# Kernel optimization log

Measured on AMD Instinct MI355X. Metric: run time of the kernel, lower is better.

## Reference

```python
import jax, jax.numpy as jnp
import numpy as np
import math

B, N, K, M = 8, 512, 128, 100

def _lin(k, fi, fo):
    kw, kb = jax.random.split(k)
    return (jax.random.normal(kw, (fi, fo), jnp.float32) / np.sqrt(fi).astype(np.float32),
            jax.random.normal(kb, (fo,), jnp.float32) * 0.01)

def setup_inputs() -> dict:
    key = jax.random.key(0)
    ks = jax.random.split(key, 10)
    xyz = jax.random.uniform(ks[0], (B, N, K, 3), jnp.float32, minval=0.5, maxval=2.8)
    counts = jax.random.randint(ks[1], (B, N), 32, K + 1)
    # padded neighbor list: valid neighbors first (flag=1), padding zeros after -> break == mask
    flags = (jnp.arange(K)[None, None, :] < counts[:, :, None]).astype(jnp.float32)
    image_dR = jnp.concatenate([xyz, flags[..., None]], axis=-1)  # [B,N,K,4]
    ew0, eb0 = _lin(ks[2], 1, 25)
    ew1, eb1 = _lin(ks[3], 25, 50)
    ew2, eb2 = _lin(ks[4], 50, M)
    fw0, fb0 = _lin(ks[5], 16 * M, 240)
    fw1, fb1 = _lin(ks[6], 240, 240)
    fw2, fb2 = _lin(ks[7], 240, 240)
    fw3, fb3 = _lin(ks[8], 240, 1)
    return dict(image_dR=image_dR, ew0=ew0, eb0=eb0, ew1=ew1, eb1=eb1, ew2=ew2, eb2=eb2,
                fw0=fw0, fb0=fb0, fw1=fw1, fb1=fb1, fw2=fw2, fb2=fb2, fw3=fw3, fb3=fb3)

def reference(image_dR, ew0, eb0, ew1, eb1, ew2, eb2, fw0, fb0, fw1, fb1, fw2, fb2, fw3, fb3):
    list_neigh = image_dR[..., 3]            # [B,N,K] neighbor flag
    xyz = image_dR[..., :3]                  # [B,N,K,3]
    Rij = jnp.sum(xyz * xyz, axis=-1)        # NOTE: original overwrites sqrt -> squared distance
    mask = list_neigh > 0
    lt10 = Rij < 10.0
    b1 = mask & lt10
    b2 = (~lt10) & (Rij < 25.0)              # cosine branch ignores mask (faithful)
    safe = jnp.where(Rij == 0.0, 1.0, Rij)
    S = jnp.where(b1, 1.0 / safe,
                  jnp.where(b2, 0.5 * jnp.cos(math.pi * (Rij - 10.0) / 15.0) + 0.5, 0.0))
    coef = jnp.where(mask, S / safe, 0.0)    # per-neighbor scaling for xyz channels
    Ri = jnp.concatenate([S[..., None], coef[..., None] * xyz], axis=-1)  # [B,N,K,4]
    # embedding net on scalar S_Rij
    h = jnp.tanh(S[..., None] @ ew0 + eb0)
    h = jnp.tanh(h @ ew1 + eb1)
    G = jnp.tanh(h @ ew2 + eb2)              # [B,N,K,M]
    G16 = G[..., :16]
    tmpA = jnp.einsum('bnjm,bnjf->bnmf', G16, Ri)   # [B,N,16,4]
    tmpB = jnp.einsum('bnjf,bnjm->bnfm', Ri, G)     # [B,N,4,M]
    DR = jnp.einsum('bnmf,bnfh->bnmh', tmpA, tmpB).reshape(image_dR.shape[0], image_dR.shape[1], -1)
    h = jnp.tanh(DR @ fw0 + fb0)
    h = jnp.tanh(h @ fw1 + fb1)
    h = jnp.tanh(h @ fw2 + fb2)
    Ei = h @ fw3 + fb3                       # [B,N,1]
    Etot = jnp.sum(Ei, axis=1)               # [B,1]
    return Etot, Ei
```

## Files before the change

### kernel.cpp

```cpp
#include <hip/hip_runtime.h>
#include <hip/hip_bf16.h>
#include <math.h>

#define B_ 8
#define N_ 512
#define K_ 128
#define M_ 100
#define NPAIR (B_*N_)
#define DRLEN 1600
#define F0 240
#define NPAD 256

#define NLUT 2048
#define LUT2_STRIDE 128
#define SMAX 1.5f
#define EPB 8

using bf16x8 = __attribute__((ext_vector_type(8))) __bf16;
using f32x4  = __attribute__((ext_vector_type(4))) float;

static __device__ __forceinline__ float tanh_f(float x){
  float xc = fminf(fmaxf(x, -15.f), 15.f);
  float e = __expf(2.f*xc);
  return __fdividef(e - 1.f, e + 1.f);
}

#define W0T_BLOCKS 100
#define SMALL_ELEMS (2*NPAD*NPAD + 3*NPAD)
#define SMALL_BLOCKS ((SMALL_ELEMS + 255)/256)
#define LUT_BLOCKS (NLUT/EPB)

__global__ __launch_bounds__(256) void prep_fused(
    const float* __restrict__ fw0, const float* __restrict__ fw1,
    const float* __restrict__ fw2,
    const float* __restrict__ fb0, const float* __restrict__ fb1,
    const float* __restrict__ fb2,
    const float* __restrict__ ew0, const float* __restrict__ eb0,
    const float* __restrict__ ew1, const float* __restrict__ eb1,
    const float* __restrict__ ew2, const float* __restrict__ eb2,
    __hip_bfloat16* __restrict__ W0T, __hip_bfloat16* __restrict__ W1T,
    __hip_bfloat16* __restrict__ W2T,
    float* __restrict__ b0p, float* __restrict__ b1p, float* __restrict__ b2p,
    float2* __restrict__ T2)
{
  __shared__ float tile[64][65];
  __shared__ float sh0[EPB][26];
  __shared__ float sh1[EPB][52];
  const int bb = blockIdx.x;
  const int t = threadIdx.x;

  if (bb < W0T_BLOCKS){
    const int k0 = (bb % 25) * 64;
    const int n0 = (bb / 25) * 64;
    const int tc = t & 63, tr = t >> 6;
    #pragma unroll
    for (int i = 0; i < 16; i++){
      int r = i*4 + tr;
      int n = n0 + tc;
      tile[r][tc] = (n < F0) ? fw0[(size_t)(k0 + r)*F0 + n] : 0.f;
    }
    __syncthreads();
    #pragma unroll
    for (int i = 0; i < 16; i++){
      int r = i*4 + tr;
      W0T[(size_t)(n0 + r)*DRLEN + k0 + tc] = __float2bfloat16(tile[tc][r]);
    }
  } else if (bb < W0T_BLOCKS + SMALL_BLOCKS){
    int idx = (bb - W0T_BLOCKS)*256 + t;
    if (idx < NPAD*NPAD){
      int n = idx / NPAD, k = idx % NPAD;
      W1T[idx] = __float2bfloat16((n < F0 && k < F0) ? fw1[(size_t)k*F0 + n] : 0.f);
    } else if (idx < 2*NPAD*NPAD){
      int j = idx - NPAD*NPAD;
      int n = j / NPAD, k = j % NPAD;
      W2T[j] = __float2bfloat16((n < F0 && k < F0) ? fw2[(size_t)k*F0 + n] : 0.f);
    } else if (idx < SMALL_ELEMS){
      int j = idx - 2*NPAD*NPAD;
      int which = j / NPAD, c = j % NPAD;
      const float* s = (which == 0) ? fb0 : (which == 1) ? fb1 : fb2;
      float* d = (which == 0) ? b0p : (which == 1) ? b1p : b2p;
      d[c] = (c < F0) ? s[c] : 0.f;
    }
  } else {
    const int e0 = (bb - W0T_BLOCKS - SMALL_BLOCKS) * EPB;
    if (t < EPB*25){
      int e = t / 25, c = t % 25;
      float S = (float)(e0 + e) * (SMAX / (float)(NLUT - 1));
      sh0[e][c] = tanh_f(fmaf(S, ew0[c], eb0[c]));
    }
    __syncthreads();
    for (int o = t; o < EPB*50; o += 256){
      int e = o / 50, c = o % 50;
      float a = eb1[c], b = 0.f;
      #pragma unroll
      for (int k = 0; k < 24; k += 2){
        a = fmaf(sh0[e][k],   ew1[k*50 + c],     a);
        b = fmaf(sh0[e][k+1], ew1[(k+1)*50 + c], b);
      }
      a = fmaf(sh0[e][24], ew1[24*50 + c], a);
      sh1[e][c] = tanh_f(a + b);
    }
    __syncthreads();
    for (int o = t; o < EPB*M_; o += 256){
      int e = o / M_, c = o % M_;
      float a = eb2[c], b = 0.f;
      #pragma unroll
      for (int k = 0; k < 50; k += 2){
        a = fmaf(sh1[e][k],   ew2[k*M_ + c],     a);
        b = fmaf(sh1[e][k+1], ew2[(k+1)*M_ + c], b);
      }
      float g = tanh_f(a + b);
      int ge = e0 + e;
      T2[(size_t)ge*LUT2_STRIDE + c].x = g;
      if (ge > 0)
        T2[(size_t)(ge-1)*LUT2_STRIDE + c].y = g;
    }
  }
}

__global__ __launch_bounds__(128) void embed_kernel(
    const float* __restrict__ img, const float2* __restrict__ T2,
    __hip_bfloat16* __restrict__ DR)
{
  __shared__ float4 sRi[K_];
  __shared__ int    sJ[K_];
  __shared__ float  sW[K_];
  __shared__ float  sB[4][M_];

  const int pair = blockIdx.x;
  const int t = threadIdx.x;

  {
    float4 v = *(const float4*)(img + ((size_t)pair*K_ + t)*4);
    float x = v.x, y = v.y, z = v.z, fl = v.w;
    float R = fmaf(x, x, fmaf(y, y, z*z));
    bool mask = fl > 0.f;
    bool lt10 = R < 10.f;
    float safe = (R == 0.f) ? 1.f : R;
    float Sc = 0.5f*cosf(0.20943951023931953f*(R - 10.f)) + 0.5f;
    float S;
    if (mask && lt10)            S = 1.f/safe;
    else if (!lt10 && R < 25.f)  S = Sc;
    else                         S = 0.f;
    float coef = mask ? S/safe : 0.f;
    sRi[t] = make_float4(S, coef*x, coef*y, coef*z);

    float fidx = fminf(S, SMAX) * ((float)(NLUT - 1) / SMAX);
    float fi = floorf(fidx);
    int i = (int)fi;
    float w = fidx - fi;
    if (i > NLUT - 2){ i = NLUT - 2; w = 1.f; }
    sJ[t] = i * LUT2_STRIDE;
    sW[t] = w;
  }
  __syncthreads();

  if (t < M_){
    const int m = t;
    float a0[4] = {0.f,0.f,0.f,0.f};
    float a1[4] = {0.f,0.f,0.f,0.f};
    for (int j = 0; j < K_; j += 8){
      float2 tv[8];
      #pragma unroll
      for (int u = 0; u < 8; u++) tv[u] = T2[sJ[j+u] + m];
      #pragma unroll
      for (int u = 0; u < 8; u++){
        float g = fmaf(sW[j+u], tv[u].y - tv[u].x, tv[u].x);
        float4 ri = sRi[j+u];
        if ((u & 1) == 0){
          a0[0] = fmaf(ri.x, g, a0[0]);
          a0[1] = fmaf(ri.y, g, a0[1]);
          a0[2] = fmaf(ri.z, g, a0[2]);
          a0[3] = fmaf(ri.w, g, a0[3]);
        } else {
          a1[0] = fmaf(ri.x, g, a1[0]);
          a1[1] = fmaf(ri.y, g, a1[1]);
          a1[2] = fmaf(ri.z, g, a1[2]);
          a1[3] = fmaf(ri.w, g, a1[3]);
        }
      }
    }
    sB[0][m] = a0[0] + a1[0];
    sB[1][m] = a0[1] + a1[1];
    sB[2][m] = a0[2] + a1[2];
    sB[3][m] = a0[3] + a1[3];
  }
  __syncthreads();

  __hip_bfloat16* drp = DR + (size_t)pair*DRLEN;
  for (int o = t; o < DRLEN; o += 128){
    int m = o / M_, h = o % M_;
    float d = sB[0][m]*sB[0][h] + sB[1][m]*sB[1][h]
            + sB[2][m]*sB[2][h] + sB[3][m]*sB[3][h];
    drp[o] = __float2bfloat16(d);
  }
}

template<int KK, int NITER>
__global__ __launch_bounds__(256) void gemm_lds(
    const __hip_bfloat16* __restrict__ A_, const __hip_bfloat16* __restrict__ Bt_,
    const float* __restrict__ bias, __hip_bfloat16* __restrict__ Y)
{
  __shared__ __align__(16) __bf16 As[2][64][72];
  __shared__ __align__(16) __bf16 Bs[2][64][72];

  const __bf16* A  = (const __bf16*)A_;
  const __bf16* Bt = (const __bf16*)Bt_;
  const int tid = threadIdx.x;
  const int lane = tid & 63, wave = tid >> 6;
  const int wm = wave & 1, wn = wave >> 1;
  const int l15 = lane & 15, q = lane >> 4;
  const int row0 = blockIdx.x * 64;
  const int col0 = blockIdx.y * 64;

  int arow[2], ac8[2]; size_t aoff[2], boff[2];
  #pragma unroll
  for (int i = 0; i < 2; i++){
    int cid = tid + i*256; arow[i] = cid >> 3; ac8[i] = cid & 7;
    aoff[i] = (size_t)(row0 + arow[i])*KK + ac8[i]*8;
    boff[i] = (size_t)(col0 + arow[i])*KK + ac8[i]*8;
  }

  bf16x8 Ar[2][2], Br[2][2];

  #pragma unroll
  for (int i = 0; i < 2; i++) Ar[0][i] = *(const bf16x8*)(A + aoff[i]);
  #pragma unroll
  for (int i = 0; i < 2; i++) Br[0][i] = *(const bf16x8*)(Bt + boff[i]);
  #pragma unroll
  for (int i = 0; i < 2; i++) *(bf16x8*)&As[0][arow[i]][ac8[i]*8] = Ar[0][i];
  #pragma unroll
  for (int i = 0; i < 2; i++) *(bf16x8*)&Bs[0][arow[i]][ac8[i]*8] = Br[0][i];
  #pragma unroll
  for (int i = 0; i < 2; i++) Ar[1][i] = *(const bf16x8*)(A + aoff[i] + 64);
  #pragma unroll
  for (int i = 0; i < 2; i++) Br[1][i] = *(const bf16x8*)(Bt + boff[i] + 64);
  __syncthreads();

  f32x4 acc[2][2] = {};

  #pragma unroll
  for (int it = 0; it < NITER; it++){
    const int buf = it & 1;
    #pragma unroll
    for (int ks = 0; ks < 2; ks++){
      bf16x8 a0 = *(const bf16x8*)&As[buf][wm*32 +      l15][ks*32 + q*8];
      bf16x8 a1 = *(const bf16x8*)&As[buf][wm*32 + 16 + l15][ks*32 + q*8];
      bf16x8 b0 = *(const bf16x8*)&Bs[buf][wn*32 +      l15][ks*32 + q*8];
      bf16x8 b1 = *(const bf16x8*)&Bs[buf][wn*32 + 16 + l15][ks*32 + q*8];
      acc[0][0] = __builtin_amdgcn_mfma_f32_16x16x32_bf16(a0, b0, acc[0][0], 0,0,0);
      acc[1][0] = __builtin_amdgcn_mfma_f32_16x16x32_bf16(a1, b0, acc[1][0], 0,0,0);
      acc[0][1] = __builtin_amdgcn_mfma_f32_16x16x32_bf16(a0, b1, acc[0][1], 0,0,0);
      acc[1][1] = __builtin_amdgcn_mfma_f32_16x16x32_bf16(a1, b1, acc[1][1], 0,0,0);
    }
    if (it + 1 < NITER){
      const int nb = buf ^ 1;
      const int set = (it + 1) & 1;
      #pragma unroll
      for (int i = 0; i < 2; i++) *(bf16x8*)&As[nb][arow[i]][ac8[i]*8] = Ar[set][i];
      #pragma unroll
      for (int i = 0; i < 2; i++) *(bf16x8*)&Bs[nb][arow[i]][ac8[i]*8] = Br[set][i];
      if (it + 2 < NITER){
        const int s2 = it & 1;
        const size_t k2 = (size_t)(it + 2) * 64;
        #pragma unroll
        for (int i = 0; i < 2; i++) Ar[s2][i] = *(const bf16x8*)(A + aoff[i] + k2);
        #pragma unroll
        for (int i = 0; i < 2; i++) Br[s2][i] = *(const bf16x8*)(Bt + boff[i] + k2);
      }
      __syncthreads();
    }
  }

  #pragma unroll
  for (int i = 0; i < 2; i++){
    #pragma unroll
    for (int j = 0; j < 2; j++){
      int c = col0 + wn*32 + j*16 + l15;
      float bs = bias[c];
      #pragma unroll
      for (int r = 0; r < 4; r++){
        int rr = row0 + wm*32 + i*16 + q*4 + r;
        float v = tanh_f(acc[i][j][r] + bs);
        Y[(size_t)rr*NPAD + c] = __float2bfloat16(v);
      }
    }
  }
}

__global__ __launch_bounds__(256) void gemv_out(
    const __hip_bfloat16* __restrict__ H, const float* __restrict__ w3,
    const float* __restrict__ b3, float* __restrict__ Ei,
    float* __restrict__ outEi)
{
  int row  = (blockIdx.x * 256 + threadIdx.x) >> 6;
  int lane = threadIdx.x & 63;
  const __hip_bfloat16* hp = H + (size_t)row * NPAD;
  float a = 0.f;
  for (int k = lane; k < F0; k += 64) a = fmaf(__bfloat162float(hp[k]), w3[k], a);
  #pragma unroll
  for (int off = 32; off; off >>= 1) a += __shfl_down(a, off, 64);
  if (lane == 0){
    float e = a + b3[0];
    Ei[row] = e;
    outEi[row] = e;
  }
}

__global__ __launch_bounds__(256) void etot_k(
    const float* __restrict__ Ei, float* __restrict__ outE)
{
  int b = blockIdx.x;
  int t = threadIdx.x;
  float s = Ei[b*N_ + t] + Ei[b*N_ + 256 + t];
  #pragma unroll
  for (int off = 32; off; off >>= 1) s += __shfl_down(s, off, 64);
  __shared__ float ws[4];
  if ((t & 63) == 0) ws[t >> 6] = s;
  __syncthreads();
  if (t == 0) outE[b] = ws[0] + ws[1] + ws[2] + ws[3];
}

extern "C" void kernel_launch(void* const* d_in, const int* in_sizes, int n_in,
                              void* d_out, int out_size, void* d_ws, size_t ws_size,
                              hipStream_t stream)
{
  const float* img = (const float*)d_in[0];
  const float* ew0 = (const float*)d_in[1];
  const float* eb0 = (const float*)d_in[2];
  const float* ew1 = (const float*)d_in[3];
  const float* eb1 = (const float*)d_in[4];
  const float* ew2 = (const float*)d_in[5];
  const float* eb2 = (const float*)d_in[6];
  const float* fw0 = (const float*)d_in[7];
  const float* fb0 = (const float*)d_in[8];
  const float* fw1 = (const float*)d_in[9];
  const float* fb1 = (const float*)d_in[10];
  const float* fw2 = (const float*)d_in[11];
  const float* fb2 = (const float*)d_in[12];
  const float* fw3 = (const float*)d_in[13];
  const float* fb3 = (const float*)d_in[14];

  char* w = (char*)d_ws;
  __hip_bfloat16* DRb = (__hip_bfloat16*)(w);
  __hip_bfloat16* H1b = (__hip_bfloat16*)(w + 13107200);
  __hip_bfloat16* H2b = (__hip_bfloat16*)(w + 15204352);
  __hip_bfloat16* H3b = (__hip_bfloat16*)(w + 17301504);
  __hip_bfloat16* W0T = (__hip_bfloat16*)(w + 19398656);
  __hip_bfloat16* W1T = (__hip_bfloat16*)(w + 20217856);
  __hip_bfloat16* W2T = (__hip_bfloat16*)(w + 20348928);
  float* b0p = (float*)(w + 20480000);
  float* b1p = (float*)(w + 20481024);
  float* b2p = (float*)(w + 20482048);
  float2* LUT2 = (float2*)(w + 20483072);
  float* Ei  = (float*)(w + 22580224);

  float* out = (float*)d_out;

  prep_fused<<<W0T_BLOCKS + SMALL_BLOCKS + LUT_BLOCKS, 256, 0, stream>>>(
      fw0, fw1, fw2, fb0, fb1, fb2,
      ew0, eb0, ew1, eb1, ew2, eb2,
      W0T, W1T, W2T, b0p, b1p, b2p, LUT2);

  embed_kernel<<<NPAIR, 128, 0, stream>>>(img, LUT2, DRb);

  dim3 gg(NPAIR/64, NPAD/64);
  gemm_lds<DRLEN, 25><<<gg, 256, 0, stream>>>(DRb, W0T, b0p, H1b);
  gemm_lds<NPAD,   4><<<gg, 256, 0, stream>>>(H1b, W1T, b1p, H2b);
  gemm_lds<NPAD,   4><<<gg, 256, 0, stream>>>(H2b, W2T, b2p, H3b);

  gemv_out<<<NPAIR/4, 256, 0, stream>>>(H3b, fw3, fb3, Ei, out + 8);
  etot_k<<<B_, 256, 0, stream>>>(Ei, out);
}
```

Measured before the change: 150.3 us.

## Fuse fitting layers two and three, output GEMV and energy sum into one kernel

Replaces the two 240x240 GEMM launches, the output GEMV and the per-batch reduction with a single kernel. Each block keeps a 16-row activation tile in LDS, runs both hidden layers with MFMA and double-buffered weight staging, then dots the result with the final weights and atomically adds into Etot (zeroed in the prep kernel). This removes three launches and the global round trips of the intermediate activations. In exchange each block re-streams the full W1/W2 weights for only 16 rows and uses one wave row-tile, so reuse is low, and the float atomics make the summation order nondeterministic.

```diff
diff --git a/kernel.cpp b/kernel.cpp
--- a/kernel.cpp
+++ b/kernel.cpp
@@ -25,23 +25,30 @@
   return __fdividef(e - 1.f, e + 1.f);
 }
 
+static __device__ __forceinline__ __bf16 f2b(float v){
+  __hip_bfloat16 h = __float2bfloat16(v);
+  return *reinterpret_cast<__bf16*>(&h);
+}
+
 #define W0T_BLOCKS 100
-#define SMALL_ELEMS (2*NPAD*NPAD + 3*NPAD)
+#define N2 (2*NPAD*NPAD)
+#define SMALL_ELEMS (N2 + 4*NPAD + 9)
 #define SMALL_BLOCKS ((SMALL_ELEMS + 255)/256)
 #define LUT_BLOCKS (NLUT/EPB)
 
 __global__ __launch_bounds__(256) void prep_fused(
     const float* __restrict__ fw0, const float* __restrict__ fw1,
-    const float* __restrict__ fw2,
+    const float* __restrict__ fw2, const float* __restrict__ fw3,
     const float* __restrict__ fb0, const float* __restrict__ fb1,
-    const float* __restrict__ fb2,
+    const float* __restrict__ fb2, const float* __restrict__ fb3,
     const float* __restrict__ ew0, const float* __restrict__ eb0,
     const float* __restrict__ ew1, const float* __restrict__ eb1,
     const float* __restrict__ ew2, const float* __restrict__ eb2,
     __hip_bfloat16* __restrict__ W0T, __hip_bfloat16* __restrict__ W1T,
     __hip_bfloat16* __restrict__ W2T,
     float* __restrict__ b0p, float* __restrict__ b1p, float* __restrict__ b2p,
-    float2* __restrict__ T2)
+    float* __restrict__ w3p, float* __restrict__ b3s,
+    float* __restrict__ out, float2* __restrict__ T2)
 {
   __shared__ float tile[64][65];
   __shared__ float sh0[EPB][26];
@@ -70,16 +77,22 @@
     if (idx < NPAD*NPAD){
       int n = idx / NPAD, k = idx % NPAD;
       W1T[idx] = __float2bfloat16((n < F0 && k < F0) ? fw1[(size_t)k*F0 + n] : 0.f);
-    } else if (idx < 2*NPAD*NPAD){
+    } else if (idx < N2){
       int j = idx - NPAD*NPAD;
       int n = j / NPAD, k = j % NPAD;
       W2T[j] = __float2bfloat16((n < F0 && k < F0) ? fw2[(size_t)k*F0 + n] : 0.f);
-    } else if (idx < SMALL_ELEMS){
-      int j = idx - 2*NPAD*NPAD;
-      int which = j / NPAD, c = j % NPAD;
-      const float* s = (which == 0) ? fb0 : (which == 1) ? fb1 : fb2;
-      float* d = (which == 0) ? b0p : (which == 1) ? b1p : b2p;
-      d[c] = (c < F0) ? s[c] : 0.f;
+    } else if (idx < N2 + NPAD){
+      int c = idx - N2;            b0p[c] = (c < F0) ? fb0[c] : 0.f;
+    } else if (idx < N2 + 2*NPAD){
+      int c = idx - N2 - NPAD;     b1p[c] = (c < F0) ? fb1[c] : 0.f;
+    } else if (idx < N2 + 3*NPAD){
+      int c = idx - N2 - 2*NPAD;   b2p[c] = (c < F0) ? fb2[c] : 0.f;
+    } else if (idx < N2 + 4*NPAD){
+      int c = idx - N2 - 3*NPAD;   w3p[c] = (c < F0) ? fw3[c] : 0.f;
+    } else if (idx == N2 + 4*NPAD){
+      b3s[0] = fb3[0];
+    } else if (idx < N2 + 4*NPAD + 9){
+      out[idx - (N2 + 4*NPAD + 1)] = 0.f;
     }
   } else {
     const int e0 = (bb - W0T_BLOCKS - SMALL_BLOCKS) * EPB;
@@ -288,37 +301,104 @@
   }
 }
 
-__global__ __launch_bounds__(256) void gemv_out(
-    const __hip_bfloat16* __restrict__ H, const float* __restrict__ w3,
-    const float* __restrict__ b3, float* __restrict__ Ei,
-    float* __restrict__ outEi)
+__global__ __launch_bounds__(256) void fit23(
+    const __hip_bfloat16* __restrict__ H1_,
+    const __hip_bfloat16* __restrict__ W1T_, const __hip_bfloat16* __restrict__ W2T_,
+    const float* __restrict__ b1p, const float* __restrict__ b2p,
+    const float* __restrict__ w3p, const float* __restrict__ b3s,
+    float* __restrict__ out)
 {
-  int row  = (blockIdx.x * 256 + threadIdx.x) >> 6;
-  int lane = threadIdx.x & 63;
-  const __hip_bfloat16* hp = H + (size_t)row * NPAD;
-  float a = 0.f;
-  for (int k = lane; k < F0; k += 64) a = fmaf(__bfloat162float(hp[k]), w3[k], a);
-  #pragma unroll
-  for (int off = 32; off; off >>= 1) a += __shfl_down(a, off, 64);
-  if (lane == 0){
-    float e = a + b3[0];
-    Ei[row] = e;
-    outEi[row] = e;
-  }
-}
-
-__global__ __launch_bounds__(256) void etot_k(
-    const float* __restrict__ Ei, float* __restrict__ outE)
-{
-  int b = blockIdx.x;
-  int t = threadIdx.x;
-  float s = Ei[b*N_ + t] + Ei[b*N_ + 256 + t];
-  #pragma unroll
-  for (int off = 32; off; off >>= 1) s += __shfl_down(s, off, 64);
-  __shared__ float ws[4];
-  if ((t & 63) == 0) ws[t >> 6] = s;
-  __syncthreads();
-  if (t == 0) outE[b] = ws[0] + ws[1] + ws[2] + ws[3];
+  __shared__ __align__(16) __bf16 Hs[16][268];
+  __shared__ __align__(16) __bf16 Bs[2][256][36];
+  __shared__ float sEi[4][16];
+
+  const __bf16* H1  = (const __bf16*)H1_;
+  const int tid = threadIdx.x;
+  const int lane = tid & 63, wave = tid >> 6;
+  const int l15 = lane & 15, q = lane >> 4;
+  const int r0 = blockIdx.x * 16;
+  const int wc0 = wave * 64;
+
+  #pragma unroll
+  for (int i = 0; i < 2; i++){
+    int c = tid + i*256;
+    int row = c >> 5, c8 = c & 31;
+    *(bf16x8*)&Hs[row][c8*8] = *(const bf16x8*)(H1 + (size_t)(r0 + row)*NPAD + c8*8);
+  }
+
+  auto stageB = [&](const __bf16* Bt, int k0, int buf){
+    #pragma unroll
+    for (int i = 0; i < 4; i++){
+      int c = tid + i*256;
+      int n = c >> 2, k8 = c & 3;
+      *(bf16x8*)&Bs[buf][n][k8*8] = *(const bf16x8*)(Bt + (size_t)n*NPAD + k0 + k8*8);
+    }
+  };
+
+  for (int layer = 0; layer < 2; layer++){
+    const __bf16* Bt  = (layer == 0) ? (const __bf16*)W1T_ : (const __bf16*)W2T_;
+    const float* bias = (layer == 0) ? b1p : b2p;
+
+    f32x4 acc[4] = {};
+    stageB(Bt, 0, 0);
+    __syncthreads();
+
+    for (int it = 0; it < 8; it++){
+      const int buf = it & 1;
+      const int k0 = it * 32;
+      bf16x8 a = *(const bf16x8*)&Hs[l15][k0 + q*8];
+      #pragma unroll
+      for (int tnum = 0; tnum < 4; tnum++){
+        bf16x8 b = *(const bf16x8*)&Bs[buf][wc0 + tnum*16 + l15][q*8];
+        acc[tnum] = __builtin_amdgcn_mfma_f32_16x16x32_bf16(a, b, acc[tnum], 0,0,0);
+      }
+      if (it + 1 < 8) stageB(Bt, (it+1)*32, buf ^ 1);
+      __syncthreads();
+    }
+
+    if (layer == 0){
+      #pragma unroll
+      for (int tnum = 0; tnum < 4; tnum++){
+        int col = wc0 + tnum*16 + l15;
+        float bs = bias[col];
+        #pragma unroll
+        for (int r = 0; r < 4; r++)
+          Hs[q*4 + r][col] = f2b(tanh_f(acc[tnum][r] + bs));
+      }
+      __syncthreads();
+    } else {
+      float part[4] = {0.f,0.f,0.f,0.f};
+      #pragma unroll
+      for (int tnum = 0; tnum < 4; tnum++){
+        int col = wc0 + tnum*16 + l15;
+        float bs = bias[col];
+        float wv = w3p[col];
+        #pragma unroll
+        for (int r = 0; r < 4; r++){
+          float h = tanh_f(acc[tnum][r] + bs);
+          part[r] = fmaf(h, wv, part[r]);
+        }
+      }
+      #pragma unroll
+      for (int off = 1; off < 16; off <<= 1){
+        #pragma unroll
+        for (int r = 0; r < 4; r++) part[r] += __shfl_xor(part[r], off, 64);
+      }
+      if (l15 == 0){
+        #pragma unroll
+        for (int r = 0; r < 4; r++) sEi[wave][q*4 + r] = part[r];
+      }
+      __syncthreads();
+      if (tid < 16){
+        float e = sEi[0][tid] + sEi[1][tid] + sEi[2][tid] + sEi[3][tid] + b3s[0];
+        out[8 + r0 + tid] = e;
+        float v = e;
+        #pragma unroll
+        for (int off = 1; off < 16; off <<= 1) v += __shfl_xor(v, off, 64);
+        if (tid == 0) atomicAdd(&out[r0 >> 9], v);
+      }
+    }
+  }
 }
 
 extern "C" void kernel_launch(void* const* d_in, const int* in_sizes, int n_in,
@@ -344,31 +424,27 @@
   char* w = (char*)d_ws;
   __hip_bfloat16* DRb = (__hip_bfloat16*)(w);
   __hip_bfloat16* H1b = (__hip_bfloat16*)(w + 13107200);
-  __hip_bfloat16* H2b = (__hip_bfloat16*)(w + 15204352);
-  __hip_bfloat16* H3b = (__hip_bfloat16*)(w + 17301504);
-  __hip_bfloat16* W0T = (__hip_bfloat16*)(w + 19398656);
-  __hip_bfloat16* W1T = (__hip_bfloat16*)(w + 20217856);
-  __hip_bfloat16* W2T = (__hip_bfloat16*)(w + 20348928);
-  float* b0p = (float*)(w + 20480000);
-  float* b1p = (float*)(w + 20481024);
-  float* b2p = (float*)(w + 20482048);
-  float2* LUT2 = (float2*)(w + 20483072);
-  float* Ei  = (float*)(w + 22580224);
+  __hip_bfloat16* W0T = (__hip_bfloat16*)(w + 15204352);
+  __hip_bfloat16* W1T = (__hip_bfloat16*)(w + 16023552);
+  __hip_bfloat16* W2T = (__hip_bfloat16*)(w + 16154624);
+  float* b0p = (float*)(w + 16285696);
+  float* b1p = (float*)(w + 16286720);
+  float* b2p = (float*)(w + 16287744);
+  float* w3p = (float*)(w + 16288768);
+  float* b3s = (float*)(w + 16289792);
+  float2* LUT2 = (float2*)(w + 16290816);
 
   float* out = (float*)d_out;
 
   prep_fused<<<W0T_BLOCKS + SMALL_BLOCKS + LUT_BLOCKS, 256, 0, stream>>>(
-      fw0, fw1, fw2, fb0, fb1, fb2,
+      fw0, fw1, fw2, fw3, fb0, fb1, fb2, fb3,
       ew0, eb0, ew1, eb1, ew2, eb2,
-      W0T, W1T, W2T, b0p, b1p, b2p, LUT2);
+      W0T, W1T, W2T, b0p, b1p, b2p, w3p, b3s, out, LUT2);
 
   embed_kernel<<<NPAIR, 128, 0, stream>>>(img, LUT2, DRb);
 
   dim3 gg(NPAIR/64, NPAD/64);
   gemm_lds<DRLEN, 25><<<gg, 256, 0, stream>>>(DRb, W0T, b0p, H1b);
-  gemm_lds<NPAD,   4><<<gg, 256, 0, stream>>>(H1b, W1T, b1p, H2b);
-  gemm_lds<NPAD,   4><<<gg, 256, 0, stream>>>(H2b, W2T, b2p, H3b);
-
-  gemv_out<<<NPAIR/4, 256, 0, stream>>>(H3b, fw3, fb3, Ei, out + 8);
-  etot_k<<<B_, 256, 0, stream>>>(Ei, out);
-}
+
+  fit23<<<NPAIR/16, 256, 0, stream>>>(H1b, W1T, W2T, b1p, b2p, w3p, b3s, out);
+}
```

New measurement: 150.9 us. Within noise of the previous version (+0.4%).
